# Kernel optimization log

Measured on AMD Instinct MI355X. Metric: run time of the kernel, lower is better.

## Reference

```python
import jax, jax.numpy as jnp
import numpy as np

REPEAT = 75  # upsample_repeat
UP = 4       # upsample_convs[0]


def setup_inputs() -> dict:
    key = jax.random.key(0)
    ks = jax.random.split(key, 12)
    B, L, F = 4, 48, 80
    C, H, A = 256, 896, 256  # conditional_size, rnn_size, signal_channels
    T = L * UP * REPEAT
    def xav(k, shape, fan_in):
        return jax.random.normal(k, shape, jnp.float32) * (1.0 / np.sqrt(fan_in))
    return {
        "local_features": jax.random.normal(ks[0], (B, L, F), jnp.float32),
        "gold_signal": jax.random.uniform(ks[1], (B, T), jnp.float32, -1.0, 1.0),
        "proj_w": xav(ks[2], (C, F), F),
        "proj_b": jnp.zeros((C,), jnp.float32),
        "up_w": xav(ks[3], (C, C, UP), C),
        "up_b": jnp.zeros((C,), jnp.float32),
        "embed_w": xav(ks[4], (C,), 1),
        "embed_b": jnp.zeros((C,), jnp.float32),
        "gru_wi": xav(ks[5], (3 * H, C), C),
        "gru_wh": xav(ks[6], (3 * H, H), H),
        "gru_bi": jnp.zeros((3 * H,), jnp.float32),
        "gru_bh": jnp.zeros((3 * H,), jnp.float32),
        "out_w1": xav(ks[7], (H, H), H),
        "out_b1": jnp.zeros((H,), jnp.float32),
        "out_w2": xav(ks[8], (A, H), H),
        "out_b2": jnp.zeros((A,), jnp.float32),
    }


def _forward(local_features, gold_signal, proj_w, proj_b, up_w, up_b,
             embed_w, embed_b, gru_wi, gru_wh, gru_bi, gru_bh,
             out_w1, out_b1, out_w2, out_b2):
    B = local_features.shape[0]
    O = up_w.shape[0]
    # --- conditional feature upsample ---
    # 1x1 conv: [B,L,F] -> [B,C,L]
    x = jnp.einsum("blf,cf->bcl", local_features, proj_w) + proj_b[None, :, None]
    # transposed conv, kernel=stride=UP: [B,C,L] -> [B,C,L*UP]
    x = jnp.einsum("bcl,ock->bolk", x, up_w).reshape(B, O, -1) + up_b[None, :, None]
    cond = jnp.repeat(x, REPEAT, axis=2)  # [B,C,T]
    # --- embed gold signal (1x1 conv, in_channels=1) ---
    sig = gold_signal[:, None, :] * embed_w[None, :, None] + embed_b[None, :, None]
    feats = (sig + cond).transpose(2, 0, 1)  # [T,B,C]
    # --- GRU (torch semantics), precompute input projections ---
    xp = feats @ gru_wi.T + gru_bi  # [T,B,3H]
    H = gru_wh.shape[1]

    def step(h, xpt):
        gh = h @ gru_wh.T + gru_bh
        xr, xz, xn = jnp.split(xpt, 3, axis=-1)
        hr, hz, hn = jnp.split(gh, 3, axis=-1)
        r = jax.nn.sigmoid(xr + hr)
        z = jax.nn.sigmoid(xz + hz)
        n = jnp.tanh(xn + r * hn)
        h_new = (1.0 - z) * n + z * h
        return h_new, h_new

    h0 = jnp.zeros((B, H), feats.dtype)
    _, hs = jax.lax.scan(step, h0, xp)  # [T,B,H]
    # --- output MLP + log-softmax over channels ---
    y = jax.nn.relu(hs @ out_w1.T + out_b1)
    logits = y @ out_w2.T + out_b2  # [T,B,A]
    logp = jax.nn.log_softmax(logits, axis=2)
    return logp.transpose(1, 2, 0)  # [B,A,T]


def reference(local_features, gold_signal, proj_w, proj_b, up_w, up_b,
              embed_w, embed_b, gru_wi, gru_wh, gru_bi, gru_bh,
              out_w1, out_b1, out_w2, out_b2):
    return _forward(local_features, gold_signal, proj_w, proj_b, up_w, up_b,
                    embed_w, embed_b, gru_wi, gru_wh, gru_bi, gru_bh,
                    out_w1, out_b1, out_w2, out_b2)
```

## Files before the change

kernel.cpp:

```cpp
#include <hip/hip_runtime.h>
#include <hip/hip_bf16.h>

#define B_ 4
#define L_ 48
#define F_ 80
#define C_ 256
#define H_ 896
#define G3_ 2688
#define A_ 256
#define T_ 14400
#define NBLK_ 192
#define REP_ 75

#define NMEM 28
#define RPW 12

typedef _Float16 __attribute__((ext_vector_type(8))) f16x8;
typedef __attribute__((ext_vector_type(4))) float f32x4;
typedef _Float16 __attribute__((ext_vector_type(2))) half2_;

__device__ __forceinline__ float fdot2f16(unsigned int a, unsigned int b, float c){
  return __builtin_amdgcn_fdot2(__builtin_bit_cast(half2_, a), __builtin_bit_cast(half2_, b), c, false);
}
__device__ __forceinline__ unsigned short f2h(float x){
  return __builtin_bit_cast(unsigned short, (_Float16)x);
}
__device__ __forceinline__ unsigned int packh2(float a, float b){
  return (unsigned int)f2h(a) | ((unsigned int)f2h(b) << 16);
}

template<int CTRL>
__device__ __forceinline__ float dppadd(float x){
  int r = __builtin_amdgcn_update_dpp(0, __builtin_bit_cast(int, x), CTRL, 0xF, 0xF, true);
  return x + __builtin_bit_cast(float, r);
}
__device__ __forceinline__ float wred(float x){
  x = dppadd<0xB1>(x);
  x = dppadd<0x4E>(x);
  x = dppadd<0x124>(x);
  x = dppadd<0x128>(x);
  x = dppadd<0x142>(x);
  x = dppadd<0x143>(x);
  return x;
}

__device__ __forceinline__ void ld7_llc(const unsigned int* base, unsigned int* hd){
  asm volatile(
    "global_load_dword %0, %7, off sc0 sc1\n\t"
    "global_load_dword %1, %7, off offset:256 sc0 sc1\n\t"
    "global_load_dword %2, %7, off offset:512 sc0 sc1\n\t"
    "global_load_dword %3, %7, off offset:768 sc0 sc1\n\t"
    "global_load_dword %4, %7, off offset:1024 sc0 sc1\n\t"
    "global_load_dword %5, %7, off offset:1280 sc0 sc1\n\t"
    "global_load_dword %6, %7, off offset:1536 sc0 sc1\n\t"
    "s_waitcnt vmcnt(0)"
    : "=&v"(hd[0]), "=&v"(hd[1]), "=&v"(hd[2]), "=&v"(hd[3]),
      "=&v"(hd[4]), "=&v"(hd[5]), "=&v"(hd[6])
    : "v"(base)
    : "memory");
}

__global__ void k_transpose_pw(const float* __restrict__ pw, float* __restrict__ pwT){
  int idx = blockIdx.x * 256 + threadIdx.x;
  if (idx >= F_ * C_) return;
  int f = idx / C_, c = idx % C_;
  pwT[idx] = pw[c * F_ + f];
}

__global__ void k_x1(const float* __restrict__ lf, const float* __restrict__ pwT,
                     const float* __restrict__ pb, float* __restrict__ x1){
  int bl = blockIdx.x;
  int c = threadIdx.x;
  const float* lrow = lf + (size_t)bl * F_;
  float acc = pb[c];
  for (int f = 0; f < F_; ++f) acc = fmaf(lrow[f], pwT[f * C_ + c], acc);
  x1[(size_t)bl * C_ + c] = acc;
}

__global__ void k_transpose_up(const float* __restrict__ up, float* __restrict__ upT){
  int idx = blockIdx.x * 256 + threadIdx.x;
  int o = idx % C_, c = (idx / C_) % C_, k = idx / (C_ * C_);
  upT[idx] = up[(o * C_ + c) * 4 + k];
}

__global__ void k_cond(const float* __restrict__ upT, const float* __restrict__ x1,
                       const float* __restrict__ ub, float* __restrict__ cond){
  int bblk = blockIdx.x;
  int blk = bblk % NBLK_;
  int b = bblk / NBLK_;
  int l = blk >> 2, kk = blk & 3;
  int o = threadIdx.x;
  const float* x1row = x1 + ((size_t)b * L_ + l) * C_;
  const float* uT = upT + (size_t)kk * C_ * C_;
  float acc = ub[o];
  for (int c = 0; c < C_; ++c) acc = fmaf(x1row[c], uT[c * C_ + o], acc);
  cond[(size_t)bblk * C_ + o] = acc;
}

__global__ void k_transpose_wi(const float* __restrict__ wi, float* __restrict__ wiT){
  int idx = blockIdx.x * 256 + threadIdx.x;
  int g = idx % G3_, c = idx / G3_;
  wiT[idx] = wi[(size_t)g * C_ + c];
}

__global__ void k_v(const float* __restrict__ wiT, const float* __restrict__ eb,
                    const float* __restrict__ cond, const float* __restrict__ bi,
                    float* __restrict__ v){
  int idx = blockIdx.x * 512 + threadIdx.x;
  int g = idx % G3_;
  int bblk = idx / G3_;
  const float* crow = cond + (size_t)bblk * C_;
  float acc = bi[g];
  for (int c = 0; c < C_; ++c) acc = fmaf(eb[c] + crow[c], wiT[(size_t)c * G3_ + g], acc);
  v[idx] = acc;
}

__global__ void k_u(const float* __restrict__ wiT, const float* __restrict__ ew,
                    float* __restrict__ u){
  int g = blockIdx.x * 256 + threadIdx.x;
  if (g >= G3_) return;
  float acc = 0.f;
  for (int c = 0; c < C_; ++c) acc = fmaf(ew[c], wiT[(size_t)c * G3_ + g], acc);
  u[g] = acc;
}

__global__ void k_packwh(const float* __restrict__ wh, unsigned int* __restrict__ whp){
  int idx = blockIdx.x * 256 + threadIdx.x;
  int lane = idx & 63;
  int r2 = idx >> 6;
  int dw = r2 % 7; int r3 = r2 / 7;
  int i = r3 % RPW; int W = r3 / RPW;
  int g = (i >> 2) * H_ + W * 4 + (i & 3);
  int k = dw * 128 + lane * 2;
  const float* p = wh + (size_t)g * H_ + k;
  whp[idx] = packh2(p[0], p[1]);
}

__global__ void k_cvth(const float* __restrict__ src, unsigned short* __restrict__ dst, int n){
  int idx = blockIdx.x * 256 + threadIdx.x;
  if (idx >= n) return;
  dst[idx] = f2h(src[idx]);
}

__global__ __launch_bounds__(576, 1) void k_gru(
    const float* __restrict__ gold, const float* __restrict__ v,
    const float* __restrict__ u, const float* __restrict__ bh,
    const unsigned int* __restrict__ whp,
    unsigned short* hsx)
{
  const int bid = blockIdx.x;
  const int batch = (bid & 7) >> 1;
  const int m = ((bid >> 3) << 1) | (bid & 1);
  const int tid = threadIdx.x;
  const int wave = tid >> 6;
  const int lane = tid & 63;

  __shared__ unsigned int lds_h[2][448];
  __shared__ int flags[8];

  if (tid < 8) flags[tid] = 0;
  __syncthreads();

  if (wave == 8){
    for (int t = 0; t < T_; ++t){
      const unsigned int* hp =
          (const unsigned int*)(hsx + ((size_t)t * B_ + batch) * H_) + lane;
      unsigned int pend = 0x7F;
      do {
        unsigned int hd[7];
        ld7_llc(hp, hd);
#pragma unroll
        for (int dw = 0; dw < 7; ++dw){
          if (pend & (1u << dw)){
            if (__all(hd[dw] != ~0u)){
              lds_h[t & 1][dw * 64 + lane] = hd[dw];
              asm volatile("s_waitcnt lgkmcnt(0)" ::: "memory");
              if (lane == 0)
                __hip_atomic_store(&flags[dw], t + 1, __ATOMIC_RELAXED,
                                   __HIP_MEMORY_SCOPE_WORKGROUP);
              pend &= ~(1u << dw);
            }
          }
        }
      } while (pend);
    }
    return;
  }

  const int W = m * 8 + wave;

  unsigned int wreg[RPW][7];
#pragma unroll
  for (int i = 0; i < RPW; ++i){
    const unsigned int* p = whp + ((size_t)(W * RPW + i) * 7) * 64 + lane;
#pragma unroll
    for (int dw = 0; dw < 7; ++dw) wreg[i][dw] = p[dw * 64];
  }

  const bool owner = (lane >= 48) && (lane < 52);
  const int jj = lane - 48;
  const int jg = 4 * W + (jj & 3);
  float u3[3] = {0,0,0}, bh3[3] = {0,0,0}, v3[3] = {0,0,0}, v3n[3] = {0,0,0};
  float hcur = 0.f;
  if (owner){
    u3[0] = u[jg]; u3[1] = u[jg + H_]; u3[2] = u[jg + 2 * H_];
    bh3[0] = bh[jg]; bh3[1] = bh[jg + H_]; bh3[2] = bh[jg + 2 * H_];
    const float* vp = v + ((size_t)(batch * NBLK_)) * G3_ + jg;
    v3[0] = vp[0]; v3[1] = vp[H_]; v3[2] = vp[2 * H_];
  }
  const float* goldb = gold + (size_t)batch * T_;
  int cnt = 0, blkc = 0;

  for (int t = 0; t < T_; ++t){
    float go = goldb[t];

    float acc[RPW];
#pragma unroll
    for (int i = 0; i < RPW; ++i) acc[i] = 0.f;

#pragma unroll
    for (int dw = 0; dw < 7; ++dw){
      while (__hip_atomic_load(&flags[dw], __ATOMIC_RELAXED,
                               __HIP_MEMORY_SCOPE_WORKGROUP) < t + 1) {}
      unsigned int hdw = lds_h[t & 1][dw * 64 + lane];
#pragma unroll
      for (int i = 0; i < RPW; ++i) acc[i] = fdot2f16(wreg[i][dw], hdw, acc[i]);
    }

#pragma unroll
    for (int i = 0; i < RPW; ++i) acc[i] = wred(acc[i]);

    if (owner){
      if (cnt == REP_ - 2){
        int nb = blkc + 1; if (nb > NBLK_ - 1) nb = NBLK_ - 1;
        const float* vp = v + ((size_t)(batch * NBLK_ + nb)) * G3_ + jg;
        v3n[0] = vp[0]; v3n[1] = vp[H_]; v3n[2] = vp[2 * H_];
      }
      float hr = jj==0 ? acc[0] : jj==1 ? acc[1] : jj==2 ? acc[2]  : acc[3];
      float hz = jj==0 ? acc[4] : jj==1 ? acc[5] : jj==2 ? acc[6]  : acc[7];
      float hn = jj==0 ? acc[8] : jj==1 ? acc[9] : jj==2 ? acc[10] : acc[11];
      hr += bh3[0]; hz += bh3[1]; hn += bh3[2];
      float xr = fmaf(go, u3[0], v3[0]);
      float xz = fmaf(go, u3[1], v3[1]);
      float xn = fmaf(go, u3[2], v3[2]);
      float r = 1.f / (1.f + __expf(-(xr + hr)));
      float z = 1.f / (1.f + __expf(-(xz + hz)));
      float e = __expf(2.f * (xn + r * hn));
      float n = 1.f - 2.f / (e + 1.f);
      float hnew = (1.f - z) * n + z * hcur;
      hcur = hnew;
      unsigned int h16 = (unsigned int)f2h(hnew);
      unsigned int oth = (unsigned int)__builtin_amdgcn_update_dpp(
          0, (int)h16, 0xB1, 0xF, 0xF, true);
      unsigned int packed = h16 | (oth << 16);
      unsigned int p23 = (unsigned int)__builtin_amdgcn_update_dpp(
          0, (int)packed, 0x4E, 0xF, 0xF, true);
      if (jj == 0){
        unsigned long long v64 = (unsigned long long)packed
                               | ((unsigned long long)p23 << 32);
        unsigned long long* dst =
            (unsigned long long*)((unsigned int*)(hsx + ((size_t)(t + 1) * B_ + batch) * H_)
                                  + 2 * W);
        __hip_atomic_store(dst, v64, __ATOMIC_RELAXED, __HIP_MEMORY_SCOPE_AGENT);
      }
    }
    if (++cnt == REP_){
      cnt = 0; ++blkc;
      v3[0] = v3n[0]; v3[1] = v3n[1]; v3[2] = v3n[2];
    }
  }
}

__global__ __launch_bounds__(256) void k_mlp(
    const unsigned short* hs, const unsigned short* __restrict__ w1h,
    const unsigned short* __restrict__ w2h, const float* __restrict__ ob1,
    const float* __restrict__ ob2, float* logits)
{
  const int mtile = blockIdx.x * 32;
  const int tid = threadIdx.x;
  const int wid = tid >> 6, lane = tid & 63;
  const int l15 = lane & 15, l4 = lane >> 4;
  __shared__ unsigned short y_lds[32 * 904];

  for (int nblk = 0; nblk < 14; ++nblk){
    f32x4 acc[2] = {(f32x4)(0.f), (f32x4)(0.f)};
    const int colg = nblk * 64 + wid * 16 + l15;
    for (int kk = 0; kk < 28; ++kk){
      const int k = kk * 32 + l4 * 8;
      f16x8 bfrag = *(const f16x8*)(w1h + (size_t)colg * H_ + k);
#pragma unroll
      for (int mf = 0; mf < 2; ++mf){
        f16x8 afrag = *(const f16x8*)(hs + (size_t)(mtile + mf * 16 + l15) * H_ + k);
        acc[mf] = __builtin_amdgcn_mfma_f32_16x16x32_f16(afrag, bfrag, acc[mf], 0, 0, 0);
      }
    }
    float bias = ob1[colg];
#pragma unroll
    for (int mf = 0; mf < 2; ++mf)
#pragma unroll
      for (int rg = 0; rg < 4; ++rg){
        float yv = acc[mf][rg] + bias;
        yv = yv > 0.f ? yv : 0.f;
        y_lds[(mf * 16 + l4 * 4 + rg) * 904 + colg] = f2h(yv);
      }
  }
  __syncthreads();

  f32x4 a2acc[2][4];
#pragma unroll
  for (int mf = 0; mf < 2; ++mf)
#pragma unroll
    for (int nf = 0; nf < 4; ++nf) a2acc[mf][nf] = (f32x4)(0.f);

  for (int kk = 0; kk < 28; ++kk){
    const int k = kk * 32 + l4 * 8;
    f16x8 a2[2];
#pragma unroll
    for (int mf = 0; mf < 2; ++mf)
      a2[mf] = *(const f16x8*)(&y_lds[(mf * 16 + l15) * 904 + k]);
#pragma unroll
    for (int nf = 0; nf < 4; ++nf){
      const int col = wid * 64 + nf * 16 + l15;
      f16x8 bfrag = *(const f16x8*)(w2h + (size_t)col * H_ + k);
#pragma unroll
      for (int mf = 0; mf < 2; ++mf)
        a2acc[mf][nf] = __builtin_amdgcn_mfma_f32_16x16x32_f16(a2[mf], bfrag, a2acc[mf][nf], 0, 0, 0);
    }
  }
#pragma unroll
  for (int nf = 0; nf < 4; ++nf){
    const int col = wid * 64 + nf * 16 + l15;
    const float bias = ob2[col];
#pragma unroll
    for (int mf = 0; mf < 2; ++mf)
#pragma unroll
      for (int rg = 0; rg < 4; ++rg){
        const int mrow = mtile + mf * 16 + l4 * 4 + rg;
        logits[(size_t)mrow * 448 + col] = a2acc[mf][nf][rg] + bias;
      }
  }
}

__global__ __launch_bounds__(256) void k_softmax(const float* __restrict__ logits,
                                                 float* __restrict__ out)
{
  const int bid = blockIdx.x;
  const int b = bid / 225;
  const int t0 = (bid % 225) * 64;
  const int tid = threadIdx.x;
  __shared__ float pm[64][4];
  __shared__ float ps[64][4];
  __shared__ float lz[64];
  {
    const int r = tid >> 2, q = tid & 3;
    const float* row = logits + (size_t)((t0 + r) * 4 + b) * 448 + q * 64;
    float mx = -1e30f;
    for (int j = 0; j < 64; ++j) mx = fmaxf(mx, row[j]);
    float s = 0.f;
    for (int j = 0; j < 64; ++j) s += __expf(row[j] - mx);
    pm[r][q] = mx; ps[r][q] = s;
  }
  __syncthreads();
  if (tid < 64){
    float m0 = pm[tid][0], m1 = pm[tid][1], m2 = pm[tid][2], m3 = pm[tid][3];
    float mx = fmaxf(fmaxf(m0, m1), fmaxf(m2, m3));
    float s = ps[tid][0] * __expf(m0 - mx) + ps[tid][1] * __expf(m1 - mx)
            + ps[tid][2] * __expf(m2 - mx) + ps[tid][3] * __expf(m3 - mx);
    lz[tid] = mx + logf(s);
  }
  __syncthreads();
  for (int i = 0; i < 64; ++i){
    const int idx = i * 256 + tid;
    const int a = idx >> 6, tt = idx & 63;
    float x = logits[(size_t)((t0 + tt) * 4 + b) * 448 + a];
    out[((size_t)(b * A_) + a) * T_ + t0 + tt] = x - lz[tt];
  }
}

extern "C" void kernel_launch(void* const* d_in, const int* in_sizes, int n_in,
                              void* d_out, int out_size, void* d_ws, size_t ws_size,
                              hipStream_t stream)
{
  (void)in_sizes; (void)n_in; (void)out_size; (void)ws_size;
  const float* lf   = (const float*)d_in[0];
  const float* gold = (const float*)d_in[1];
  const float* pw   = (const float*)d_in[2];
  const float* pb   = (const float*)d_in[3];
  const float* upw  = (const float*)d_in[4];
  const float* upb  = (const float*)d_in[5];
  const float* ew   = (const float*)d_in[6];
  const float* eb   = (const float*)d_in[7];
  const float* wi   = (const float*)d_in[8];
  const float* wh   = (const float*)d_in[9];
  const float* bi   = (const float*)d_in[10];
  const float* bhp  = (const float*)d_in[11];
  const float* w1   = (const float*)d_in[12];
  const float* b1   = (const float*)d_in[13];
  const float* w2   = (const float*)d_in[14];
  const float* b2   = (const float*)d_in[15];
  float* out = (float*)d_out;
  char* ws = (char*)d_ws;

  size_t off = 0;
  auto take = [&](size_t bytes){
    size_t r = off; off += (bytes + 255) & ~(size_t)255; return r;
  };
  float* pwT  = (float*)(ws + take((size_t)F_ * C_ * 4));
  float* x1   = (float*)(ws + take((size_t)B_ * L_ * C_ * 4));
  float* upT  = (float*)(ws + take((size_t)4 * C_ * C_ * 4));
  float* cond = (float*)(ws + take((size_t)B_ * NBLK_ * C_ * 4));
  float* wiT  = (float*)(ws + take((size_t)C_ * G3_ * 4));
  float* v    = (float*)(ws + take((size_t)B_ * NBLK_ * G3_ * 4));
  float* u    = (float*)(ws + take((size_t)G3_ * 4));
  unsigned int*   whp = (unsigned int*)(ws + take((size_t)224 * RPW * 7 * 64 * 4));
  unsigned short* w1h = (unsigned short*)(ws + take((size_t)H_ * H_ * 2));
  unsigned short* w2h = (unsigned short*)(ws + take((size_t)A_ * H_ * 2));
  unsigned short* hsx = (unsigned short*)(ws + take((size_t)(T_ + 1) * B_ * H_ * 2));

  hipMemsetAsync((void*)hsx, 0, (size_t)B_ * H_ * 2, stream);
  hipMemsetAsync((void*)(hsx + (size_t)B_ * H_), 0xFF, (size_t)T_ * B_ * H_ * 2, stream);

  k_transpose_pw<<<80, 256, 0, stream>>>(pw, pwT);
  k_x1<<<B_ * L_, 256, 0, stream>>>(lf, pwT, pb, x1);
  k_transpose_up<<<1024, 256, 0, stream>>>(upw, upT);
  k_cond<<<B_ * NBLK_, 256, 0, stream>>>(upT, x1, upb, cond);
  k_transpose_wi<<<2688, 256, 0, stream>>>(wi, wiT);
  k_v<<<4032, 512, 0, stream>>>(wiT, eb, cond, bi, v);
  k_u<<<11, 256, 0, stream>>>(wiT, ew, u);
  k_packwh<<<4704, 256, 0, stream>>>(wh, whp);
  k_cvth<<<(H_ * H_ + 255) / 256, 256, 0, stream>>>(w1, w1h, H_ * H_);
  k_cvth<<<(A_ * H_ + 255) / 256, 256, 0, stream>>>(w2, w2h, A_ * H_);

  k_gru<<<112, 576, 0, stream>>>(gold, v, u, bhp, whp, hsx);

  const unsigned short* hs_mlp = hsx + (size_t)B_ * H_;
  float* logits = (float*)hsx + (size_t)B_ * 448;
  k_mlp<<<1800, 256, 0, stream>>>(hs_mlp, w1h, w2h, b1, b2, logits);
  k_softmax<<<900, 256, 0, stream>>>(logits, out);
}
```

Measured before the change: 41.54 ms.

## Process all four batches per GRU block, shrinking grid to 28 blocks

```diff
diff --git a/kernel.cpp b/kernel.cpp
--- a/kernel.cpp
+++ b/kernel.cpp
@@ -44,19 +44,47 @@
   return x;
 }
 
-__device__ __forceinline__ void ld7_llc(const unsigned int* base, unsigned int* hd){
+__device__ __forceinline__ void ld28_llc(const unsigned int* p01,
+                                         const unsigned int* p23,
+                                         unsigned int* hd){
   asm volatile(
-    "global_load_dword %0, %7, off sc0 sc1\n\t"
-    "global_load_dword %1, %7, off offset:256 sc0 sc1\n\t"
-    "global_load_dword %2, %7, off offset:512 sc0 sc1\n\t"
-    "global_load_dword %3, %7, off offset:768 sc0 sc1\n\t"
-    "global_load_dword %4, %7, off offset:1024 sc0 sc1\n\t"
-    "global_load_dword %5, %7, off offset:1280 sc0 sc1\n\t"
-    "global_load_dword %6, %7, off offset:1536 sc0 sc1\n\t"
+    "global_load_dword %0,  %28, off sc0 sc1\n\t"
+    "global_load_dword %1,  %28, off offset:256 sc0 sc1\n\t"
+    "global_load_dword %2,  %28, off offset:512 sc0 sc1\n\t"
+    "global_load_dword %3,  %28, off offset:768 sc0 sc1\n\t"
+    "global_load_dword %4,  %28, off offset:1024 sc0 sc1\n\t"
+    "global_load_dword %5,  %28, off offset:1280 sc0 sc1\n\t"
+    "global_load_dword %6,  %28, off offset:1536 sc0 sc1\n\t"
+    "global_load_dword %7,  %28, off offset:1792 sc0 sc1\n\t"
+    "global_load_dword %8,  %28, off offset:2048 sc0 sc1\n\t"
+    "global_load_dword %9,  %28, off offset:2304 sc0 sc1\n\t"
+    "global_load_dword %10, %28, off offset:2560 sc0 sc1\n\t"
+    "global_load_dword %11, %28, off offset:2816 sc0 sc1\n\t"
+    "global_load_dword %12, %28, off offset:3072 sc0 sc1\n\t"
+    "global_load_dword %13, %28, off offset:3328 sc0 sc1\n\t"
+    "global_load_dword %14, %29, off sc0 sc1\n\t"
+    "global_load_dword %15, %29, off offset:256 sc0 sc1\n\t"
+    "global_load_dword %16, %29, off offset:512 sc0 sc1\n\t"
+    "global_load_dword %17, %29, off offset:768 sc0 sc1\n\t"
+    "global_load_dword %18, %29, off offset:1024 sc0 sc1\n\t"
+    "global_load_dword %19, %29, off offset:1280 sc0 sc1\n\t"
+    "global_load_dword %20, %29, off offset:1536 sc0 sc1\n\t"
+    "global_load_dword %21, %29, off offset:1792 sc0 sc1\n\t"
+    "global_load_dword %22, %29, off offset:2048 sc0 sc1\n\t"
+    "global_load_dword %23, %29, off offset:2304 sc0 sc1\n\t"
+    "global_load_dword %24, %29, off offset:2560 sc0 sc1\n\t"
+    "global_load_dword %25, %29, off offset:2816 sc0 sc1\n\t"
+    "global_load_dword %26, %29, off offset:3072 sc0 sc1\n\t"
+    "global_load_dword %27, %29, off offset:3328 sc0 sc1\n\t"
     "s_waitcnt vmcnt(0)"
-    : "=&v"(hd[0]), "=&v"(hd[1]), "=&v"(hd[2]), "=&v"(hd[3]),
-      "=&v"(hd[4]), "=&v"(hd[5]), "=&v"(hd[6])
-    : "v"(base)
+    : "=&v"(hd[0]),  "=&v"(hd[1]),  "=&v"(hd[2]),  "=&v"(hd[3]),
+      "=&v"(hd[4]),  "=&v"(hd[5]),  "=&v"(hd[6]),  "=&v"(hd[7]),
+      "=&v"(hd[8]),  "=&v"(hd[9]),  "=&v"(hd[10]), "=&v"(hd[11]),
+      "=&v"(hd[12]), "=&v"(hd[13]), "=&v"(hd[14]), "=&v"(hd[15]),
+      "=&v"(hd[16]), "=&v"(hd[17]), "=&v"(hd[18]), "=&v"(hd[19]),
+      "=&v"(hd[20]), "=&v"(hd[21]), "=&v"(hd[22]), "=&v"(hd[23]),
+      "=&v"(hd[24]), "=&v"(hd[25]), "=&v"(hd[26]), "=&v"(hd[27])
+    : "v"(p01), "v"(p23)
     : "memory");
 }
 
@@ -148,37 +176,42 @@
     const unsigned int* __restrict__ whp,
     unsigned short* hsx)
 {
-  const int bid = blockIdx.x;
-  const int batch = (bid & 7) >> 1;
-  const int m = ((bid >> 3) << 1) | (bid & 1);
+  const int m = blockIdx.x;
   const int tid = threadIdx.x;
   const int wave = tid >> 6;
   const int lane = tid & 63;
 
-  __shared__ unsigned int lds_h[2][448];
-  __shared__ int flags[8];
-
-  if (tid < 8) flags[tid] = 0;
+  __shared__ unsigned int lds_h[B_][2][448];
+  __shared__ int flags[B_];
+
+  if (tid < B_) flags[tid] = 0;
   __syncthreads();
 
   if (wave == 8){
     for (int t = 0; t < T_; ++t){
-      const unsigned int* hp =
-          (const unsigned int*)(hsx + ((size_t)t * B_ + batch) * H_) + lane;
-      unsigned int pend = 0x7F;
+      const unsigned int* base =
+          (const unsigned int*)(hsx + ((size_t)t * B_) * H_) + lane;
+      const unsigned int* p01 = base;
+      const unsigned int* p23 = base + 896;
+      unsigned int pend = 0xF;
       do {
-        unsigned int hd[7];
-        ld7_llc(hp, hd);
-#pragma unroll
-        for (int dw = 0; dw < 7; ++dw){
-          if (pend & (1u << dw)){
-            if (__all(hd[dw] != ~0u)){
-              lds_h[t & 1][dw * 64 + lane] = hd[dw];
+        unsigned int hd[28];
+        ld28_llc(p01, p23, hd);
+#pragma unroll
+        for (int b = 0; b < B_; ++b){
+          if (pend & (1u << b)){
+            bool ok = true;
+#pragma unroll
+            for (int dw = 0; dw < 7; ++dw) ok &= (hd[b * 7 + dw] != ~0u);
+            if (__all(ok)){
+#pragma unroll
+              for (int dw = 0; dw < 7; ++dw)
+                lds_h[b][t & 1][dw * 64 + lane] = hd[b * 7 + dw];
               asm volatile("s_waitcnt lgkmcnt(0)" ::: "memory");
               if (lane == 0)
-                __hip_atomic_store(&flags[dw], t + 1, __ATOMIC_RELAXED,
+                __hip_atomic_store(&flags[b], t + 1, __ATOMIC_RELEASE,
                                    __HIP_MEMORY_SCOPE_WORKGROUP);
-              pend &= ~(1u << dw);
+              pend &= ~(1u << b);
             }
           }
         }
@@ -200,74 +233,75 @@
   const bool owner = (lane >= 48) && (lane < 52);
   const int jj = lane - 48;
   const int jg = 4 * W + (jj & 3);
-  float u3[3] = {0,0,0}, bh3[3] = {0,0,0}, v3[3] = {0,0,0}, v3n[3] = {0,0,0};
-  float hcur = 0.f;
+  float u3[3] = {0,0,0}, bh3[3] = {0,0,0};
+  float v3[B_][3];
+  float hcur[B_] = {0.f, 0.f, 0.f, 0.f};
   if (owner){
     u3[0] = u[jg]; u3[1] = u[jg + H_]; u3[2] = u[jg + 2 * H_];
     bh3[0] = bh[jg]; bh3[1] = bh[jg + H_]; bh3[2] = bh[jg + 2 * H_];
-    const float* vp = v + ((size_t)(batch * NBLK_)) * G3_ + jg;
-    v3[0] = vp[0]; v3[1] = vp[H_]; v3[2] = vp[2 * H_];
-  }
-  const float* goldb = gold + (size_t)batch * T_;
+  }
   int cnt = 0, blkc = 0;
 
   for (int t = 0; t < T_; ++t){
-    float go = goldb[t];
-
-    float acc[RPW];
-#pragma unroll
-    for (int i = 0; i < RPW; ++i) acc[i] = 0.f;
-
-#pragma unroll
-    for (int dw = 0; dw < 7; ++dw){
-      while (__hip_atomic_load(&flags[dw], __ATOMIC_RELAXED,
-                               __HIP_MEMORY_SCOPE_WORKGROUP) < t + 1) {}
-      unsigned int hdw = lds_h[t & 1][dw * 64 + lane];
-#pragma unroll
-      for (int i = 0; i < RPW; ++i) acc[i] = fdot2f16(wreg[i][dw], hdw, acc[i]);
+    float go[B_];
+    if (owner){
+#pragma unroll
+      for (int b = 0; b < B_; ++b) go[b] = gold[(size_t)b * T_ + t];
     }
 
 #pragma unroll
-    for (int i = 0; i < RPW; ++i) acc[i] = wred(acc[i]);
-
-    if (owner){
-      if (cnt == REP_ - 2){
-        int nb = blkc + 1; if (nb > NBLK_ - 1) nb = NBLK_ - 1;
-        const float* vp = v + ((size_t)(batch * NBLK_ + nb)) * G3_ + jg;
-        v3n[0] = vp[0]; v3n[1] = vp[H_]; v3n[2] = vp[2 * H_];
+    for (int b = 0; b < B_; ++b){
+      while (__hip_atomic_load(&flags[b], __ATOMIC_ACQUIRE,
+                               __HIP_MEMORY_SCOPE_WORKGROUP) < t + 1)
+        __builtin_amdgcn_s_sleep(1);
+
+      float acc[RPW];
+#pragma unroll
+      for (int i = 0; i < RPW; ++i) acc[i] = 0.f;
+#pragma unroll
+      for (int dw = 0; dw < 7; ++dw){
+        unsigned int hdw = lds_h[b][t & 1][dw * 64 + lane];
+#pragma unroll
+        for (int i = 0; i < RPW; ++i) acc[i] = fdot2f16(wreg[i][dw], hdw, acc[i]);
       }
-      float hr = jj==0 ? acc[0] : jj==1 ? acc[1] : jj==2 ? acc[2]  : acc[3];
-      float hz = jj==0 ? acc[4] : jj==1 ? acc[5] : jj==2 ? acc[6]  : acc[7];
-      float hn = jj==0 ? acc[8] : jj==1 ? acc[9] : jj==2 ? acc[10] : acc[11];
-      hr += bh3[0]; hz += bh3[1]; hn += bh3[2];
-      float xr = fmaf(go, u3[0], v3[0]);
-      float xz = fmaf(go, u3[1], v3[1]);
-      float xn = fmaf(go, u3[2], v3[2]);
-      float r = 1.f / (1.f + __expf(-(xr + hr)));
-      float z = 1.f / (1.f + __expf(-(xz + hz)));
-      float e = __expf(2.f * (xn + r * hn));
-      float n = 1.f - 2.f / (e + 1.f);
-      float hnew = (1.f - z) * n + z * hcur;
-      hcur = hnew;
-      unsigned int h16 = (unsigned int)f2h(hnew);
-      unsigned int oth = (unsigned int)__builtin_amdgcn_update_dpp(
-          0, (int)h16, 0xB1, 0xF, 0xF, true);
-      unsigned int packed = h16 | (oth << 16);
-      unsigned int p23 = (unsigned int)__builtin_amdgcn_update_dpp(
-          0, (int)packed, 0x4E, 0xF, 0xF, true);
-      if (jj == 0){
-        unsigned long long v64 = (unsigned long long)packed
-                               | ((unsigned long long)p23 << 32);
-        unsigned long long* dst =
-            (unsigned long long*)((unsigned int*)(hsx + ((size_t)(t + 1) * B_ + batch) * H_)
-                                  + 2 * W);
-        __hip_atomic_store(dst, v64, __ATOMIC_RELAXED, __HIP_MEMORY_SCOPE_AGENT);
+#pragma unroll
+      for (int i = 0; i < RPW; ++i) acc[i] = wred(acc[i]);
+
+      if (owner){
+        if (cnt == 0){
+          const float* vp = v + ((size_t)(b * NBLK_ + blkc)) * G3_ + jg;
+          v3[b][0] = vp[0]; v3[b][1] = vp[H_]; v3[b][2] = vp[2 * H_];
+        }
+        float hr = jj==0 ? acc[0] : jj==1 ? acc[1] : jj==2 ? acc[2]  : acc[3];
+        float hz = jj==0 ? acc[4] : jj==1 ? acc[5] : jj==2 ? acc[6]  : acc[7];
+        float hn = jj==0 ? acc[8] : jj==1 ? acc[9] : jj==2 ? acc[10] : acc[11];
+        hr += bh3[0]; hz += bh3[1]; hn += bh3[2];
+        float xr = fmaf(go[b], u3[0], v3[b][0]);
+        float xz = fmaf(go[b], u3[1], v3[b][1]);
+        float xn = fmaf(go[b], u3[2], v3[b][2]);
+        float r = 1.f / (1.f + __expf(-(xr + hr)));
+        float z = 1.f / (1.f + __expf(-(xz + hz)));
+        float e = __expf(2.f * (xn + r * hn));
+        float n = 1.f - 2.f / (e + 1.f);
+        float hnew = (1.f - z) * n + z * hcur[b];
+        hcur[b] = hnew;
+        unsigned int h16 = (unsigned int)f2h(hnew);
+        unsigned int oth = (unsigned int)__builtin_amdgcn_update_dpp(
+            0, (int)h16, 0xB1, 0xF, 0xF, true);
+        unsigned int packed = h16 | (oth << 16);
+        unsigned int p23v = (unsigned int)__builtin_amdgcn_update_dpp(
+            0, (int)packed, 0x4E, 0xF, 0xF, true);
+        if (jj == 0){
+          unsigned long long v64 = (unsigned long long)packed
+                                 | ((unsigned long long)p23v << 32);
+          unsigned long long* dst =
+              (unsigned long long*)((unsigned int*)(hsx + ((size_t)(t + 1) * B_ + b) * H_)
+                                    + 2 * W);
+          __hip_atomic_store(dst, v64, __ATOMIC_RELAXED, __HIP_MEMORY_SCOPE_AGENT);
+        }
       }
     }
-    if (++cnt == REP_){
-      cnt = 0; ++blkc;
-      v3[0] = v3n[0]; v3[1] = v3n[1]; v3[2] = v3n[2];
-    }
+    if (++cnt == REP_){ cnt = 0; ++blkc; }
   }
 }
 
@@ -431,7 +465,7 @@
   k_cvth<<<(H_ * H_ + 255) / 256, 256, 0, stream>>>(w1, w1h, H_ * H_);
   k_cvth<<<(A_ * H_ + 255) / 256, 256, 0, stream>>>(w2, w2h, A_ * H_);
 
-  k_gru<<<112, 576, 0, stream>>>(gold, v, u, bhp, whp, hsx);
+  k_gru<<<NMEM, 576, 0, stream>>>(gold, v, u, bhp, whp, hsx);
 
   const unsigned short* hs_mlp = hsx + (size_t)B_ * H_;
   float* logits = (float*)hsx + (size_t)B_ * 448;
```

Measured after the change: 70.12 ms. 1.69x slower.
